# Performance work log

Hardware: AMD Instinct MI355X
Metric: run time of the kernel (lower is better)

Reference implementation:

```python
import jax, jax.numpy as jnp
import numpy as np

B, N, F = 4, 4096, 32
NG = 14  # number of gate graph-convs in GCNLSTM_Cell with memory state


def setup_inputs() -> dict:
    key = jax.random.key(0)
    ks = jax.random.split(key, 7)
    x = jax.random.normal(ks[0], (B, N, F), jnp.float32)
    h = jax.random.normal(ks[1], (B, N, F), jnp.float32)
    c = jax.random.normal(ks[2], (B, N, F), jnp.float32)
    m = jax.random.normal(ks[3], (B, N, F), jnp.float32)
    # weighted dense adjacency, scaled so row sums are O(1)
    adj = jax.random.uniform(ks[4], (N, N), jnp.float32) / N
    # 14 WeightedGraphConv layers: Dense F -> 2F (single FeedForward layer, no relu)
    W = jax.random.normal(ks[5], (NG, F, 2 * F), jnp.float32) * (1.0 / np.sqrt(F))
    b = jnp.zeros((NG, 2 * F), jnp.float32)
    return {"x": x, "h": h, "c": c, "m": m, "adj": adj, "W": W, "b": b}


def _gcn(ax, W, b):
    # ax: [B,N,F] = adj @ state (precomputed); Dense to 2F then GLU split.
    z = ax @ W + b  # [B,N,2F]
    ls, rs = jnp.split(z, 2, axis=-1)
    return ls * jax.nn.sigmoid(rs)


def reference(x, h, c, m, adj, W, b):
    # shared graph aggregation for x and h (adj is the same for all gates)
    ax = jnp.einsum('nm,bmf->bnf', adj, x)  # [B,N,F]
    ah = jnp.einsum('nm,bmf->bnf', adj, h)

    fx = _gcn(ax, W[0], b[0]); fh = _gcn(ah, W[1], b[1])
    ix = _gcn(ax, W[2], b[2]); ih = _gcn(ah, W[3], b[3])
    cx = _gcn(ax, W[4], b[4]); ch = _gcn(ah, W[5], b[5])
    ox = _gcn(ax, W[6], b[6]); oh = _gcn(ah, W[7], b[7])

    f = jax.nn.sigmoid(fx + fh)
    i = jax.nn.sigmoid(ix + ih)
    o = jax.nn.sigmoid(ox + oh)
    c_new = f * c + i * jnp.tanh(cx + ch)
    h1 = o * jnp.tanh(c_new)

    # memory-state block (6 more graph convs on h1 and m)
    ah1 = jnp.einsum('nm,bmf->bnf', adj, h1)
    am = jnp.einsum('nm,bmf->bnf', adj, m)
    sa_ih = _gcn(ah1, W[8], b[8]);  sa_im = _gcn(am, W[9], b[9])
    sa_gh = _gcn(ah1, W[10], b[10]); sa_gm = _gcn(am, W[11], b[11])
    sa_oh = _gcn(ah1, W[12], b[12]); sa_om = _gcn(am, W[13], b[13])

    i2 = jax.nn.sigmoid(sa_ih + sa_im)
    g = jax.nn.sigmoid(sa_gh + sa_gm)
    o2 = jax.nn.sigmoid(sa_oh + sa_om)
    m_new = i2 * m + (1.0 - i2) * g
    h_new = m_new * o2
    return h_new, c_new, m_new
```

## Files before the change

kernel.cpp:

```cpp
#include <hip/hip_runtime.h>
#include <stdint.h>

typedef __attribute__((ext_vector_type(4))) float f32x4;
typedef __attribute__((ext_vector_type(8))) short s16x8;

#define BB 4
#define NN 4096
#define FF 32
#define BNF (BB*NN*FF)

typedef __attribute__((address_space(3))) void       as3_void;
typedef const __attribute__((address_space(1))) void as1_cvoid;

static __device__ __forceinline__ float bf2f(uint16_t u) {
    union { uint32_t i; float f; } v; v.i = ((uint32_t)u) << 16; return v.f;
}
static __device__ __forceinline__ uint16_t f2bf(float f) {
    union { float f; uint32_t i; } v; v.f = f;
    uint32_t r = v.i + 0x7FFFu + ((v.i >> 16) & 1u);
    return (uint16_t)(r >> 16);
}
static __device__ __forceinline__ float sig_acc(float x) { return 1.0f / (1.0f + expf(-x)); }

__global__ __launch_bounds__(256) void prep_kernel(
    const float* __restrict__ Wf, uint16_t* __restrict__ Wp,
    const float* __restrict__ x, const float* __restrict__ h,
    const float* __restrict__ m,
    uint16_t* __restrict__ P, uint16_t* __restrict__ P2)
{
    int bid = blockIdx.x;
    int t = threadIdx.x;

    if (bid < 112) {
        int idx = bid * 256 + t;
        int g   = idx >> 11;
        int k   = (idx >> 6) & 31;
        int col = idx & 63;
        uint16_t v = f2bf(Wf[idx]);
        int gp = g >> 1;
        int sl = ((g & 1) << 2) | (k >> 3);
        int ph = sl ^ (col & 7);
        Wp[((gp * 64 + col) * 64) + ph * 8 + (k & 7)] = v;
        return;
    }
    bid -= 112;

    const float* src; uint16_t* dst; int rowbase, b, n0;
    if (bid < 512) {
        int tensor = bid >> 8;
        src = tensor ? h : x; dst = P; rowbase = tensor * 128;
        b = (bid >> 6) & 3; n0 = (bid & 63) * 64;
    } else {
        int q = bid - 512;
        src = m; dst = P2; rowbase = 128;
        b = q >> 6; n0 = (q & 63) * 64;
    }
    __shared__ uint16_t tl[32][65];
    {
        int i = t >> 2, ch = t & 3;
        size_t idx = ((size_t)(b * NN + n0 + i)) * FF + ch * 8;
        float4 v0 = *(const float4*)(src + idx);
        float4 v1 = *(const float4*)(src + idx + 4);
        uint16_t e[8] = { f2bf(v0.x), f2bf(v0.y), f2bf(v0.z), f2bf(v0.w),
                          f2bf(v1.x), f2bf(v1.y), f2bf(v1.z), f2bf(v1.w) };
        #pragma unroll
        for (int k = 0; k < 8; k++) tl[ch * 8 + k][i] = e[k];
    }
    __syncthreads();
    {
        int f = t >> 3, ch = t & 7;
        union { uint4 u; uint16_t e[8]; } v;
        #pragma unroll
        for (int k = 0; k < 8; k++) v.e[k] = tl[f][ch * 8 + k];
        size_t row = (size_t)(rowbase + b * 32 + f);
        *(uint4*)(dst + row * NN + n0 + ch * 8) = v.u;
    }
}

__global__ __launch_bounds__(256, 3) void mega1_kernel(
    const float* __restrict__ adj,
    const uint16_t* __restrict__ P,
    const uint16_t* __restrict__ Wp,
    const float* __restrict__ bf_,
    const float* __restrict__ cf,
    float* __restrict__ cnew, uint16_t* __restrict__ S2t)
{
    __shared__ __align__(16) uint16_t aLb[4][16 * 32];
    __shared__ __align__(16) uint16_t bLb[4][64 * 32];
    __shared__ float    AL[64 * 17];
    __shared__ float    SX[4][64][9];
    __shared__ uint16_t H1[32 * 18];

    int t = threadIdx.x;
    int bid = blockIdx.x;
    int b = bid >> 8, n0 = (bid & 255) * 16;
    int lane = t & 63, w = t >> 6;
    int lm = lane & 15, lk = lane >> 4;
    int j = lm, kg = lk;
    int ej = t & 15, erow = (t >> 4) & 15;

    float cv[2];
    #pragma unroll
    for (int hh = 0; hh < 2; hh++)
        cv[hh] = cf[((size_t)(b * NN + n0 + erow)) * FF + ej + hh * 16];

    int aq = t >> 6, apos = (t & 63) * 16;
    int arow = apos >> 6;
    int aslot = ((apos >> 4) & 3) ^ ((arow >> 1) & 3);
    int bpos = t * 16;
    int brow = bpos >> 6;
    int bslot = ((bpos >> 4) & 3) ^ ((brow >> 1) & 3);
    int bcrow = brow + ((brow < 32) ? b * 32 : 96 + b * 32);
    int rA = lm;          int swA = (lk ^ ((rA >> 1) & 3)) * 8;
    int rB = w * 16 + lm; int swB = (lk ^ ((rB >> 1) & 3)) * 8;

    f32x4 acc = {};
    for (int kk = 0; kk < 4096; kk += 128) {
        {
            size_t aidx = (size_t)(n0 + arow) * 4096 + kk + aq * 32 + aslot * 8;
            union { uint4 u[2]; float f[8]; } va;
            va.u[0] = *(const uint4*)(adj + aidx);
            va.u[1] = *(const uint4*)(adj + aidx + 4);
            union { uint4 u; uint16_t e[8]; } sa;
            #pragma unroll
            for (int k = 0; k < 8; k++) sa.e[k] = f2bf(va.f[k]);
            *(uint4*)((char*)aLb[aq] + apos) = sa.u;
        }
        #pragma unroll
        for (int q = 0; q < 4; q++) {
            size_t bidx = (size_t)bcrow * 4096 + kk + q * 32 + bslot * 8;
            __builtin_amdgcn_global_load_lds((as1_cvoid*)(P + bidx),
                (as3_void*)((char*)bLb[q] + bpos), 16, 0, 0);
        }
        __syncthreads();
        #pragma unroll
        for (int q = 0; q < 4; q++) {
            s16x8 af = *(const s16x8*)(aLb[q] + rA * 32 + swA);
            s16x8 bf = *(const s16x8*)(bLb[q] + rB * 32 + swB);
            acc = __builtin_amdgcn_mfma_f32_16x16x32_bf16(af, bf, acc, 0, 0, 0);
        }
        __syncthreads();
    }

    {
        int cp = w * 16 + lm;
        #pragma unroll
        for (int r = 0; r < 4; r++)
            AL[cp * 17 + lk * 4 + r] = acc[r];
    }
    __syncthreads();

    s16x8 a_ax, a_ah;
    #pragma unroll
    for (int e = 0; e < 8; e++) {
        int k = kg * 8 + e;
        a_ax[e] = (short)f2bf(AL[k * 17 + j]);
        a_ah[e] = (short)f2bf(AL[(32 + k) * 17 + j]);
    }
    {
        int p = w;
        int g0 = p * 2, g1 = p * 2 + 1;
        f32x4 ac0[4] = {}, ac1[4] = {};
        #pragma unroll
        for (int ct = 0; ct < 4; ct++) {
            int col = ct * 16 + j;
            int ph0 = (kg)     ^ (col & 7);
            int ph1 = (4 + kg) ^ (col & 7);
            s16x8 b0 = *(const s16x8*)(Wp + (p * 64 + col) * 64 + ph0 * 8);
            s16x8 b1 = *(const s16x8*)(Wp + (p * 64 + col) * 64 + ph1 * 8);
            ac0[ct] = __builtin_amdgcn_mfma_f32_16x16x32_bf16(a_ax, b0, ac0[ct], 0, 0, 0);
            ac1[ct] = __builtin_amdgcn_mfma_f32_16x16x32_bf16(a_ah, b1, ac1[ct], 0, 0, 0);
        }
        #pragma unroll
        for (int hh = 0; hh < 2; hh++)
            #pragma unroll
            for (int r = 0; r < 4; r++) {
                float z0l = ac0[hh][r]     + bf_[g0 * 64 + hh * 16 + j];
                float z0r = ac0[2 + hh][r] + bf_[g0 * 64 + 32 + hh * 16 + j];
                float z1l = ac1[hh][r]     + bf_[g1 * 64 + hh * 16 + j];
                float z1r = ac1[2 + hh][r] + bf_[g1 * 64 + 32 + hh * 16 + j];
                SX[p][lane][hh * 4 + r] = z0l * sig_acc(z0r) + z1l * sig_acc(z1r);
            }
    }
    __syncthreads();

    {
        int pl = ((erow >> 2) << 4) | ej;
        int ridx = erow & 3;
        #pragma unroll
        for (int hh = 0; hh < 2; hh++) {
            float s0 = SX[0][pl][hh * 4 + ridx];
            float s1 = SX[1][pl][hh * 4 + ridx];
            float s2 = SX[2][pl][hh * 4 + ridx];
            float s3 = SX[3][pl][hh * 4 + ridx];
            float fg = sig_acc(s0), ig = sig_acc(s1);
            float cc = tanhf(s2),   og = sig_acc(s3);
            float cn = fg * cv[hh] + ig * cc;
            size_t gidx = ((size_t)(b * NN + n0 + erow)) * FF + ej + hh * 16;
            cnew[gidx] = cn;
            H1[(ej + hh * 16) * 18 + erow] = f2bf(og * tanhf(cn));
        }
    }
    __syncthreads();
    if (t < 64) {
        int f = t >> 1, half = t & 1;
        union { uint4 u; uint16_t e[8]; } v;
        #pragma unroll
        for (int k = 0; k < 8; k++) v.e[k] = H1[f * 18 + half * 8 + k];
        *(uint4*)(S2t + ((size_t)(b * 32 + f)) * NN + n0 + half * 8) = v.u;
    }
}

__global__ __launch_bounds__(256, 3) void mega2_kernel(
    const float* __restrict__ adj,
    const uint16_t* __restrict__ P2,
    const uint16_t* __restrict__ Wp,
    const float* __restrict__ bf_,
    const float* __restrict__ mf,
    float* __restrict__ hnew, float* __restrict__ mnew)
{
    __shared__ __align__(16) uint16_t aLb[4][16 * 32];
    __shared__ __align__(16) uint16_t bLb[4][64 * 32];
    __shared__ float AL[64 * 17];
    __shared__ float SX[3][64][9];

    int t = threadIdx.x;
    int bid = blockIdx.x;
    int b = bid >> 8, n0 = (bid & 255) * 16;
    int lane = t & 63, w = t >> 6;
    int lm = lane & 15, lk = lane >> 4;
    int j = lm, kg = lk;
    int ej = t & 15, erow = (t >> 4) & 15;

    float mv[2];
    #pragma unroll
    for (int hh = 0; hh < 2; hh++)
        mv[hh] = mf[((size_t)(b * NN + n0 + erow)) * FF + ej + hh * 16];

    int aq = t >> 6, apos = (t & 63) * 16;
    int arow = apos >> 6;
    int aslot = ((apos >> 4) & 3) ^ ((arow >> 1) & 3);
    int bpos = t * 16;
    int brow = bpos >> 6;
    int bslot = ((bpos >> 4) & 3) ^ ((brow >> 1) & 3);
    int bcrow = brow + ((brow < 32) ? b * 32 : 96 + b * 32);
    int rA = lm;          int swA = (lk ^ ((rA >> 1) & 3)) * 8;
    int rB = w * 16 + lm; int swB = (lk ^ ((rB >> 1) & 3)) * 8;

    f32x4 acc = {};
    for (int kk = 0; kk < 4096; kk += 128) {
        {
            size_t aidx = (size_t)(n0 + arow) * 4096 + kk + aq * 32 + aslot * 8;
            union { uint4 u[2]; float f[8]; } va;
            va.u[0] = *(const uint4*)(adj + aidx);
            va.u[1] = *(const uint4*)(adj + aidx + 4);
            union { uint4 u; uint16_t e[8]; } sa;
            #pragma unroll
            for (int k = 0; k < 8; k++) sa.e[k] = f2bf(va.f[k]);
            *(uint4*)((char*)aLb[aq] + apos) = sa.u;
        }
        #pragma unroll
        for (int q = 0; q < 4; q++) {
            size_t bidx = (size_t)bcrow * 4096 + kk + q * 32 + bslot * 8;
            __builtin_amdgcn_global_load_lds((as1_cvoid*)(P2 + bidx),
                (as3_void*)((char*)bLb[q] + bpos), 16, 0, 0);
        }
        __syncthreads();
        #pragma unroll
        for (int q = 0; q < 4; q++) {
            s16x8 af = *(const s16x8*)(aLb[q] + rA * 32 + swA);
            s16x8 bf = *(const s16x8*)(bLb[q] + rB * 32 + swB);
            acc = __builtin_amdgcn_mfma_f32_16x16x32_bf16(af, bf, acc, 0, 0, 0);
        }
        __syncthreads();
    }

    {
        int cp = w * 16 + lm;
        #pragma unroll
        for (int r = 0; r < 4; r++)
            AL[cp * 17 + lk * 4 + r] = acc[r];
    }
    __syncthreads();

    if (w < 3) {
        s16x8 a_h1, a_m;
        #pragma unroll
        for (int e = 0; e < 8; e++) {
            int k = kg * 8 + e;
            a_h1[e] = (short)f2bf(AL[k * 17 + j]);
            a_m[e]  = (short)f2bf(AL[(32 + k) * 17 + j]);
        }
        const uint16_t* WpG = Wp + 4 * 64 * 64;
        const float*    bG  = bf_ + 512;
        int p = w;
        int g0 = p * 2, g1 = p * 2 + 1;
        f32x4 ac0[4] = {}, ac1[4] = {};
        #pragma unroll
        for (int ct = 0; ct < 4; ct++) {
            int col = ct * 16 + j;
            int ph0 = (kg)     ^ (col & 7);
            int ph1 = (4 + kg) ^ (col & 7);
            s16x8 b0 = *(const s16x8*)(WpG + (p * 64 + col) * 64 + ph0 * 8);
            s16x8 b1 = *(const s16x8*)(WpG + (p * 64 + col) * 64 + ph1 * 8);
            ac0[ct] = __builtin_amdgcn_mfma_f32_16x16x32_bf16(a_h1, b0, ac0[ct], 0, 0, 0);
            ac1[ct] = __builtin_amdgcn_mfma_f32_16x16x32_bf16(a_m, b1, ac1[ct], 0, 0, 0);
        }
        #pragma unroll
        for (int hh = 0; hh < 2; hh++)
            #pragma unroll
            for (int r = 0; r < 4; r++) {
                float z0l = ac0[hh][r]     + bG[g0 * 64 + hh * 16 + j];
                float z0r = ac0[2 + hh][r] + bG[g0 * 64 + 32 + hh * 16 + j];
                float z1l = ac1[hh][r]     + bG[g1 * 64 + hh * 16 + j];
                float z1r = ac1[2 + hh][r] + bG[g1 * 64 + 32 + hh * 16 + j];
                SX[p][lane][hh * 4 + r] = z0l * sig_acc(z0r) + z1l * sig_acc(z1r);
            }
    }
    __syncthreads();

    {
        int pl = ((erow >> 2) << 4) | ej;
        int ridx = erow & 3;
        #pragma unroll
        for (int hh = 0; hh < 2; hh++) {
            float s0 = SX[0][pl][hh * 4 + ridx];
            float s1 = SX[1][pl][hh * 4 + ridx];
            float s2 = SX[2][pl][hh * 4 + ridx];
            float i2 = sig_acc(s0);
            float gg = sig_acc(s1);
            float o2 = sig_acc(s2);
            float mn = i2 * mv[hh] + (1.0f - i2) * gg;
            size_t gidx = ((size_t)(b * NN + n0 + erow)) * FF + ej + hh * 16;
            mnew[gidx] = mn;
            hnew[gidx] = mn * o2;
        }
    }
}

extern "C" void kernel_launch(void* const* d_in, const int* in_sizes, int n_in,
                              void* d_out, int out_size, void* d_ws, size_t ws_size,
                              hipStream_t stream) {
    (void)in_sizes; (void)n_in; (void)out_size;
    const float* x   = (const float*)d_in[0];
    const float* h   = (const float*)d_in[1];
    const float* c   = (const float*)d_in[2];
    const float* m   = (const float*)d_in[3];
    const float* adj = (const float*)d_in[4];
    const float* W   = (const float*)d_in[5];
    const float* bb  = (const float*)d_in[6];
    float* out = (float*)d_out;

    char* ws = (char*)d_ws;
    uint16_t* P    = (uint16_t*)ws;
    uint16_t* P2   = (uint16_t*)(ws + (2u << 20));
    uint16_t* Wp   = (uint16_t*)(ws + (4u << 20));

    if (ws_size < (6u << 20)) return;

    prep_kernel<<<880, 256, 0, stream>>>(W, Wp, x, h, m, P, P2);

    mega1_kernel<<<1024, 256, 0, stream>>>(adj, P, Wp, bb, c, out + BNF, P2);
    mega2_kernel<<<1024, 256, 0, stream>>>(adj, P2, Wp, bb, m, out, out + 2 * BNF);
}
```

Measured before the change: 187.3 us.

## Pre-convert adjacency to bf16 once and double row tile per block

Adds a prep pass that converts the fp32 adjacency to a bf16 copy in workspace, when the workspace is large enough. Both mega kernels can then stream A with direct global-to-LDS loads instead of loading fp32 and converting in registers. Each block now covers 32 rows instead of 16, with two MFMA accumulators that share each B fragment, so the grid halves and the P reloads per row are halved. The cost is an extra 32MB write plus re-read of adjacency, fewer blocks (512) with occupancy lowered to 2 waves, and a serialized two-pass epilogue.

```diff
diff --git a/kernel.cpp b/kernel.cpp
--- a/kernel.cpp
+++ b/kernel.cpp
@@ -23,6 +23,7 @@
 static __device__ __forceinline__ float sig_acc(float x) { return 1.0f / (1.0f + expf(-x)); }
 
 __global__ __launch_bounds__(256) void prep_kernel(
+    const float* __restrict__ adj, uint16_t* __restrict__ adjb, int cvtN,
     const float* __restrict__ Wf, uint16_t* __restrict__ Wp,
     const float* __restrict__ x, const float* __restrict__ h,
     const float* __restrict__ m,
@@ -30,6 +31,18 @@
 {
     int bid = blockIdx.x;
     int t = threadIdx.x;
+
+    if (bid < cvtN) {
+        size_t i = ((size_t)bid * 256 + t) * 8;
+        float4 v0 = *(const float4*)(adj + i);
+        float4 v1 = *(const float4*)(adj + i + 4);
+        union { uint4 u; uint16_t e[8]; } o;
+        o.e[0] = f2bf(v0.x); o.e[1] = f2bf(v0.y); o.e[2] = f2bf(v0.z); o.e[3] = f2bf(v0.w);
+        o.e[4] = f2bf(v1.x); o.e[5] = f2bf(v1.y); o.e[6] = f2bf(v1.z); o.e[7] = f2bf(v1.w);
+        *(uint4*)(adjb + i) = o.u;
+        return;
+    }
+    bid -= cvtN;
 
     if (bid < 112) {
         int idx = bid * 256 + t;
@@ -77,54 +90,79 @@
     }
 }
 
-__global__ __launch_bounds__(256, 3) void mega1_kernel(
-    const float* __restrict__ adj,
+__global__ __launch_bounds__(256, 2) void mega1_kernel(
+    const void* __restrict__ Av,
     const uint16_t* __restrict__ P,
     const uint16_t* __restrict__ Wp,
     const float* __restrict__ bf_,
     const float* __restrict__ cf,
-    float* __restrict__ cnew, uint16_t* __restrict__ S2t)
+    float* __restrict__ cnew, uint16_t* __restrict__ S2t, int isf32A)
 {
-    __shared__ __align__(16) uint16_t aLb[4][16 * 32];
+    __shared__ __align__(16) uint16_t aLb[4][32 * 32];
     __shared__ __align__(16) uint16_t bLb[4][64 * 32];
-    __shared__ float    AL[64 * 17];
+    __shared__ float    AL[64 * 33];
     __shared__ float    SX[4][64][9];
     __shared__ uint16_t H1[32 * 18];
 
     int t = threadIdx.x;
     int bid = blockIdx.x;
-    int b = bid >> 8, n0 = (bid & 255) * 16;
+    int b = bid >> 7, n0 = (bid & 127) * 32;
     int lane = t & 63, w = t >> 6;
     int lm = lane & 15, lk = lane >> 4;
     int j = lm, kg = lk;
     int ej = t & 15, erow = (t >> 4) & 15;
 
-    float cv[2];
+    const uint16_t* A16 = (const uint16_t*)Av;
+    const float*    Af  = (const float*)Av;
+
+    float cv[2][2];
     #pragma unroll
-    for (int hh = 0; hh < 2; hh++)
-        cv[hh] = cf[((size_t)(b * NN + n0 + erow)) * FF + ej + hh * 16];
-
-    int aq = t >> 6, apos = (t & 63) * 16;
-    int arow = apos >> 6;
-    int aslot = ((apos >> 4) & 3) ^ ((arow >> 1) & 3);
+    for (int gh = 0; gh < 2; gh++)
+        #pragma unroll
+        for (int hh = 0; hh < 2; hh++)
+            cv[gh][hh] = cf[((size_t)(b * NN + n0 + gh * 16 + erow)) * FF + ej + hh * 16];
+
+    int aq0 = t >> 7,        ap0 = (t & 127) * 16;
+    int ar0 = ap0 >> 6,      asl0 = ((ap0 >> 4) & 3) ^ ((ar0 >> 1) & 3);
+    int gs1 = t + 256;
+    int aq1 = gs1 >> 7,      ap1 = (gs1 & 127) * 16;
+    int ar1 = ap1 >> 6,      asl1 = ((ap1 >> 4) & 3) ^ ((ar1 >> 1) & 3);
     int bpos = t * 16;
     int brow = bpos >> 6;
     int bslot = ((bpos >> 4) & 3) ^ ((brow >> 1) & 3);
     int bcrow = brow + ((brow < 32) ? b * 32 : 96 + b * 32);
-    int rA = lm;          int swA = (lk ^ ((rA >> 1) & 3)) * 8;
     int rB = w * 16 + lm; int swB = (lk ^ ((rB >> 1) & 3)) * 8;
-
-    f32x4 acc = {};
+    int swA = (lk ^ ((lm >> 1) & 3)) * 8;
+
+    f32x4 acc0 = {}, acc1 = {};
     for (int kk = 0; kk < 4096; kk += 128) {
-        {
-            size_t aidx = (size_t)(n0 + arow) * 4096 + kk + aq * 32 + aslot * 8;
-            union { uint4 u[2]; float f[8]; } va;
-            va.u[0] = *(const uint4*)(adj + aidx);
-            va.u[1] = *(const uint4*)(adj + aidx + 4);
-            union { uint4 u; uint16_t e[8]; } sa;
-            #pragma unroll
-            for (int k = 0; k < 8; k++) sa.e[k] = f2bf(va.f[k]);
-            *(uint4*)((char*)aLb[aq] + apos) = sa.u;
+        if (!isf32A) {
+            __builtin_amdgcn_global_load_lds(
+                (as1_cvoid*)(A16 + (size_t)(n0 + ar0) * 4096 + kk + aq0 * 32 + asl0 * 8),
+                (as3_void*)((char*)aLb[aq0] + ap0), 16, 0, 0);
+            __builtin_amdgcn_global_load_lds(
+                (as1_cvoid*)(A16 + (size_t)(n0 + ar1) * 4096 + kk + aq1 * 32 + asl1 * 8),
+                (as3_void*)((char*)aLb[aq1] + ap1), 16, 0, 0);
+        } else {
+            union { uint4 u; uint16_t e[8]; } sa0, sa1;
+            {
+                size_t aidx = (size_t)(n0 + ar0) * 4096 + kk + aq0 * 32 + asl0 * 8;
+                union { uint4 u[2]; float f[8]; } va;
+                va.u[0] = *(const uint4*)(Af + aidx);
+                va.u[1] = *(const uint4*)(Af + aidx + 4);
+                #pragma unroll
+                for (int k = 0; k < 8; k++) sa0.e[k] = f2bf(va.f[k]);
+            }
+            {
+                size_t aidx = (size_t)(n0 + ar1) * 4096 + kk + aq1 * 32 + asl1 * 8;
+                union { uint4 u[2]; float f[8]; } va;
+                va.u[0] = *(const uint4*)(Af + aidx);
+                va.u[1] = *(const uint4*)(Af + aidx + 4);
+                #pragma unroll
+                for (int k = 0; k < 8; k++) sa1.e[k] = f2bf(va.f[k]);
+            }
+            *(uint4*)((char*)aLb[aq0] + ap0) = sa0.u;
+            *(uint4*)((char*)aLb[aq1] + ap1) = sa1.u;
         }
         #pragma unroll
         for (int q = 0; q < 4; q++) {
@@ -135,9 +173,11 @@
         __syncthreads();
         #pragma unroll
         for (int q = 0; q < 4; q++) {
-            s16x8 af = *(const s16x8*)(aLb[q] + rA * 32 + swA);
-            s16x8 bf = *(const s16x8*)(bLb[q] + rB * 32 + swB);
-            acc = __builtin_amdgcn_mfma_f32_16x16x32_bf16(af, bf, acc, 0, 0, 0);
+            s16x8 af0 = *(const s16x8*)(aLb[q] + lm * 32 + swA);
+            s16x8 af1 = *(const s16x8*)(aLb[q] + (16 + lm) * 32 + swA);
+            s16x8 bf  = *(const s16x8*)(bLb[q] + rB * 32 + swB);
+            acc0 = __builtin_amdgcn_mfma_f32_16x16x32_bf16(af0, bf, acc0, 0, 0, 0);
+            acc1 = __builtin_amdgcn_mfma_f32_16x16x32_bf16(af1, bf, acc1, 0, 0, 0);
         }
         __syncthreads();
     }
@@ -145,119 +185,149 @@
     {
         int cp = w * 16 + lm;
         #pragma unroll
-        for (int r = 0; r < 4; r++)
-            AL[cp * 17 + lk * 4 + r] = acc[r];
+        for (int r = 0; r < 4; r++) {
+            AL[cp * 33 + lk * 4 + r]      = acc0[r];
+            AL[cp * 33 + 16 + lk * 4 + r] = acc1[r];
+        }
     }
     __syncthreads();
 
-    s16x8 a_ax, a_ah;
-    #pragma unroll
-    for (int e = 0; e < 8; e++) {
-        int k = kg * 8 + e;
-        a_ax[e] = (short)f2bf(AL[k * 17 + j]);
-        a_ah[e] = (short)f2bf(AL[(32 + k) * 17 + j]);
-    }
-    {
-        int p = w;
-        int g0 = p * 2, g1 = p * 2 + 1;
-        f32x4 ac0[4] = {}, ac1[4] = {};
-        #pragma unroll
-        for (int ct = 0; ct < 4; ct++) {
-            int col = ct * 16 + j;
-            int ph0 = (kg)     ^ (col & 7);
-            int ph1 = (4 + kg) ^ (col & 7);
-            s16x8 b0 = *(const s16x8*)(Wp + (p * 64 + col) * 64 + ph0 * 8);
-            s16x8 b1 = *(const s16x8*)(Wp + (p * 64 + col) * 64 + ph1 * 8);
-            ac0[ct] = __builtin_amdgcn_mfma_f32_16x16x32_bf16(a_ax, b0, ac0[ct], 0, 0, 0);
-            ac1[ct] = __builtin_amdgcn_mfma_f32_16x16x32_bf16(a_ah, b1, ac1[ct], 0, 0, 0);
-        }
-        #pragma unroll
-        for (int hh = 0; hh < 2; hh++)
-            #pragma unroll
-            for (int r = 0; r < 4; r++) {
-                float z0l = ac0[hh][r]     + bf_[g0 * 64 + hh * 16 + j];
-                float z0r = ac0[2 + hh][r] + bf_[g0 * 64 + 32 + hh * 16 + j];
-                float z1l = ac1[hh][r]     + bf_[g1 * 64 + hh * 16 + j];
-                float z1r = ac1[2 + hh][r] + bf_[g1 * 64 + 32 + hh * 16 + j];
-                SX[p][lane][hh * 4 + r] = z0l * sig_acc(z0r) + z1l * sig_acc(z1r);
-            }
-    }
-    __syncthreads();
-
-    {
-        int pl = ((erow >> 2) << 4) | ej;
-        int ridx = erow & 3;
-        #pragma unroll
-        for (int hh = 0; hh < 2; hh++) {
-            float s0 = SX[0][pl][hh * 4 + ridx];
-            float s1 = SX[1][pl][hh * 4 + ridx];
-            float s2 = SX[2][pl][hh * 4 + ridx];
-            float s3 = SX[3][pl][hh * 4 + ridx];
-            float fg = sig_acc(s0), ig = sig_acc(s1);
-            float cc = tanhf(s2),   og = sig_acc(s3);
-            float cn = fg * cv[hh] + ig * cc;
-            size_t gidx = ((size_t)(b * NN + n0 + erow)) * FF + ej + hh * 16;
-            cnew[gidx] = cn;
-            H1[(ej + hh * 16) * 18 + erow] = f2bf(og * tanhf(cn));
-        }
-    }
-    __syncthreads();
-    if (t < 64) {
-        int f = t >> 1, half = t & 1;
-        union { uint4 u; uint16_t e[8]; } v;
-        #pragma unroll
-        for (int k = 0; k < 8; k++) v.e[k] = H1[f * 18 + half * 8 + k];
-        *(uint4*)(S2t + ((size_t)(b * 32 + f)) * NN + n0 + half * 8) = v.u;
-    }
-}
-
-__global__ __launch_bounds__(256, 3) void mega2_kernel(
-    const float* __restrict__ adj,
+    for (int gh = 0; gh < 2; gh++) {
+        int colb = gh * 16;
+        s16x8 a_ax, a_ah;
+        #pragma unroll
+        for (int e = 0; e < 8; e++) {
+            int k = kg * 8 + e;
+            a_ax[e] = (short)f2bf(AL[k * 33 + colb + j]);
+            a_ah[e] = (short)f2bf(AL[(32 + k) * 33 + colb + j]);
+        }
+        {
+            int p = w;
+            int g0 = p * 2, g1 = p * 2 + 1;
+            f32x4 ac0[4] = {}, ac1[4] = {};
+            #pragma unroll
+            for (int ct = 0; ct < 4; ct++) {
+                int col = ct * 16 + j;
+                int ph0 = (kg)     ^ (col & 7);
+                int ph1 = (4 + kg) ^ (col & 7);
+                s16x8 b0 = *(const s16x8*)(Wp + (p * 64 + col) * 64 + ph0 * 8);
+                s16x8 b1 = *(const s16x8*)(Wp + (p * 64 + col) * 64 + ph1 * 8);
+                ac0[ct] = __builtin_amdgcn_mfma_f32_16x16x32_bf16(a_ax, b0, ac0[ct], 0, 0, 0);
+                ac1[ct] = __builtin_amdgcn_mfma_f32_16x16x32_bf16(a_ah, b1, ac1[ct], 0, 0, 0);
+            }
+            #pragma unroll
+            for (int hh = 0; hh < 2; hh++)
+                #pragma unroll
+                for (int r = 0; r < 4; r++) {
+                    float z0l = ac0[hh][r]     + bf_[g0 * 64 + hh * 16 + j];
+                    float z0r = ac0[2 + hh][r] + bf_[g0 * 64 + 32 + hh * 16 + j];
+                    float z1l = ac1[hh][r]     + bf_[g1 * 64 + hh * 16 + j];
+                    float z1r = ac1[2 + hh][r] + bf_[g1 * 64 + 32 + hh * 16 + j];
+                    SX[p][lane][hh * 4 + r] = z0l * sig_acc(z0r) + z1l * sig_acc(z1r);
+                }
+        }
+        __syncthreads();
+        {
+            int pl = ((erow >> 2) << 4) | ej;
+            int ridx = erow & 3;
+            #pragma unroll
+            for (int hh = 0; hh < 2; hh++) {
+                float s0 = SX[0][pl][hh * 4 + ridx];
+                float s1 = SX[1][pl][hh * 4 + ridx];
+                float s2 = SX[2][pl][hh * 4 + ridx];
+                float s3 = SX[3][pl][hh * 4 + ridx];
+                float fg = sig_acc(s0), ig = sig_acc(s1);
+                float cc = tanhf(s2),   og = sig_acc(s3);
+                float cn = fg * cv[gh][hh] + ig * cc;
+                size_t gidx = ((size_t)(b * NN + n0 + gh * 16 + erow)) * FF + ej + hh * 16;
+                cnew[gidx] = cn;
+                H1[(ej + hh * 16) * 18 + erow] = f2bf(og * tanhf(cn));
+            }
+        }
+        __syncthreads();
+        if (t < 64) {
+            int f = t >> 1, half = t & 1;
+            union { uint4 u; uint16_t e[8]; } v;
+            #pragma unroll
+            for (int k = 0; k < 8; k++) v.e[k] = H1[f * 18 + half * 8 + k];
+            *(uint4*)(S2t + ((size_t)(b * 32 + f)) * NN + n0 + gh * 16 + half * 8) = v.u;
+        }
+        __syncthreads();
+    }
+}
+
+__global__ __launch_bounds__(256, 2) void mega2_kernel(
+    const void* __restrict__ Av,
     const uint16_t* __restrict__ P2,
     const uint16_t* __restrict__ Wp,
     const float* __restrict__ bf_,
     const float* __restrict__ mf,
-    float* __restrict__ hnew, float* __restrict__ mnew)
+    float* __restrict__ hnew, float* __restrict__ mnew, int isf32A)
 {
-    __shared__ __align__(16) uint16_t aLb[4][16 * 32];
+    __shared__ __align__(16) uint16_t aLb[4][32 * 32];
     __shared__ __align__(16) uint16_t bLb[4][64 * 32];
-    __shared__ float AL[64 * 17];
+    __shared__ float AL[64 * 33];
     __shared__ float SX[3][64][9];
 
     int t = threadIdx.x;
     int bid = blockIdx.x;
-    int b = bid >> 8, n0 = (bid & 255) * 16;
+    int b = bid >> 7, n0 = (bid & 127) * 32;
     int lane = t & 63, w = t >> 6;
     int lm = lane & 15, lk = lane >> 4;
     int j = lm, kg = lk;
     int ej = t & 15, erow = (t >> 4) & 15;
 
-    float mv[2];
+    const uint16_t* A16 = (const uint16_t*)Av;
+    const float*    Af  = (const float*)Av;
+
+    float mv[2][2];
     #pragma unroll
-    for (int hh = 0; hh < 2; hh++)
-        mv[hh] = mf[((size_t)(b * NN + n0 + erow)) * FF + ej + hh * 16];
-
-    int aq = t >> 6, apos = (t & 63) * 16;
-    int arow = apos >> 6;
-    int aslot = ((apos >> 4) & 3) ^ ((arow >> 1) & 3);
+    for (int gh = 0; gh < 2; gh++)
+        #pragma unroll
+        for (int hh = 0; hh < 2; hh++)
+            mv[gh][hh] = mf[((size_t)(b * NN + n0 + gh * 16 + erow)) * FF + ej + hh * 16];
+
+    int aq0 = t >> 7,        ap0 = (t & 127) * 16;
+    int ar0 = ap0 >> 6,      asl0 = ((ap0 >> 4) & 3) ^ ((ar0 >> 1) & 3);
+    int gs1 = t + 256;
+    int aq1 = gs1 >> 7,      ap1 = (gs1 & 127) * 16;
+    int ar1 = ap1 >> 6,      asl1 = ((ap1 >> 4) & 3) ^ ((ar1 >> 1) & 3);
     int bpos = t * 16;
     int brow = bpos >> 6;
     int bslot = ((bpos >> 4) & 3) ^ ((brow >> 1) & 3);
     int bcrow = brow + ((brow < 32) ? b * 32 : 96 + b * 32);
-    int rA = lm;          int swA = (lk ^ ((rA >> 1) & 3)) * 8;
     int rB = w * 16 + lm; int swB = (lk ^ ((rB >> 1) & 3)) * 8;
-
-    f32x4 acc = {};
+    int swA = (lk ^ ((lm >> 1) & 3)) * 8;
+
+    f32x4 acc0 = {}, acc1 = {};
     for (int kk = 0; kk < 4096; kk += 128) {
-        {
-            size_t aidx = (size_t)(n0 + arow) * 4096 + kk + aq * 32 + aslot * 8;
-            union { uint4 u[2]; float f[8]; } va;
-            va.u[0] = *(const uint4*)(adj + aidx);
-            va.u[1] = *(const uint4*)(adj + aidx + 4);
-            union { uint4 u; uint16_t e[8]; } sa;
-            #pragma unroll
-            for (int k = 0; k < 8; k++) sa.e[k] = f2bf(va.f[k]);
-            *(uint4*)((char*)aLb[aq] + apos) = sa.u;
+        if (!isf32A) {
+            __builtin_amdgcn_global_load_lds(
+                (as1_cvoid*)(A16 + (size_t)(n0 + ar0) * 4096 + kk + aq0 * 32 + asl0 * 8),
+                (as3_void*)((char*)aLb[aq0] + ap0), 16, 0, 0);
+            __builtin_amdgcn_global_load_lds(
+                (as1_cvoid*)(A16 + (size_t)(n0 + ar1) * 4096 + kk + aq1 * 32 + asl1 * 8),
+                (as3_void*)((char*)aLb[aq1] + ap1), 16, 0, 0);
+        } else {
+            union { uint4 u; uint16_t e[8]; } sa0, sa1;
+            {
+                size_t aidx = (size_t)(n0 + ar0) * 4096 + kk + aq0 * 32 + asl0 * 8;
+                union { uint4 u[2]; float f[8]; } va;
+                va.u[0] = *(const uint4*)(Af + aidx);
+                va.u[1] = *(const uint4*)(Af + aidx + 4);
+                #pragma unroll
+                for (int k = 0; k < 8; k++) sa0.e[k] = f2bf(va.f[k]);
+            }
+            {
+                size_t aidx = (size_t)(n0 + ar1) * 4096 + kk + aq1 * 32 + asl1 * 8;
+                union { uint4 u[2]; float f[8]; } va;
+                va.u[0] = *(const uint4*)(Af + aidx);
+                va.u[1] = *(const uint4*)(Af + aidx + 4);
+                #pragma unroll
+                for (int k = 0; k < 8; k++) sa1.e[k] = f2bf(va.f[k]);
+            }
+            *(uint4*)((char*)aLb[aq0] + ap0) = sa0.u;
+            *(uint4*)((char*)aLb[aq1] + ap1) = sa1.u;
         }
         #pragma unroll
         for (int q = 0; q < 4; q++) {
@@ -268,9 +338,11 @@
         __syncthreads();
         #pragma unroll
         for (int q = 0; q < 4; q++) {
-            s16x8 af = *(const s16x8*)(aLb[q] + rA * 32 + swA);
-            s16x8 bf = *(const s16x8*)(bLb[q] + rB * 32 + swB);
-            acc = __builtin_amdgcn_mfma_f32_16x16x32_bf16(af, bf, acc, 0, 0, 0);
+            s16x8 af0 = *(const s16x8*)(aLb[q] + lm * 32 + swA);
+            s16x8 af1 = *(const s16x8*)(aLb[q] + (16 + lm) * 32 + swA);
+            s16x8 bf  = *(const s16x8*)(bLb[q] + rB * 32 + swB);
+            acc0 = __builtin_amdgcn_mfma_f32_16x16x32_bf16(af0, bf, acc0, 0, 0, 0);
+            acc1 = __builtin_amdgcn_mfma_f32_16x16x32_bf16(af1, bf, acc1, 0, 0, 0);
         }
         __syncthreads();
     }
@@ -278,63 +350,68 @@
     {
         int cp = w * 16 + lm;
         #pragma unroll
-        for (int r = 0; r < 4; r++)
-            AL[cp * 17 + lk * 4 + r] = acc[r];
+        for (int r = 0; r < 4; r++) {
+            AL[cp * 33 + lk * 4 + r]      = acc0[r];
+            AL[cp * 33 + 16 + lk * 4 + r] = acc1[r];
+        }
     }
     __syncthreads();
 
-    if (w < 3) {
-        s16x8 a_h1, a_m;
-        #pragma unroll
-        for (int e = 0; e < 8; e++) {
-            int k = kg * 8 + e;
-            a_h1[e] = (short)f2bf(AL[k * 17 + j]);
-            a_m[e]  = (short)f2bf(AL[(32 + k) * 17 + j]);
-        }
-        const uint16_t* WpG = Wp + 4 * 64 * 64;
-        const float*    bG  = bf_ + 512;
-        int p = w;
-        int g0 = p * 2, g1 = p * 2 + 1;
-        f32x4 ac0[4] = {}, ac1[4] = {};
-        #pragma unroll
-        for (int ct = 0; ct < 4; ct++) {
-            int col = ct * 16 + j;
-            int ph0 = (kg)     ^ (col & 7);
-            int ph1 = (4 + kg) ^ (col & 7);
-            s16x8 b0 = *(const s16x8*)(WpG + (p * 64 + col) * 64 + ph0 * 8);
-            s16x8 b1 = *(const s16x8*)(WpG + (p * 64 + col) * 64 + ph1 * 8);
-            ac0[ct] = __builtin_amdgcn_mfma_f32_16x16x32_bf16(a_h1, b0, ac0[ct], 0, 0, 0);
-            ac1[ct] = __builtin_amdgcn_mfma_f32_16x16x32_bf16(a_m, b1, ac1[ct], 0, 0, 0);
-        }
-        #pragma unroll
-        for (int hh = 0; hh < 2; hh++)
-            #pragma unroll
-            for (int r = 0; r < 4; r++) {
-                float z0l = ac0[hh][r]     + bG[g0 * 64 + hh * 16 + j];
-                float z0r = ac0[2 + hh][r] + bG[g0 * 64 + 32 + hh * 16 + j];
-                float z1l = ac1[hh][r]     + bG[g1 * 64 + hh * 16 + j];
-                float z1r = ac1[2 + hh][r] + bG[g1 * 64 + 32 + hh * 16 + j];
-                SX[p][lane][hh * 4 + r] = z0l * sig_acc(z0r) + z1l * sig_acc(z1r);
-            }
-    }
-    __syncthreads();
-
-    {
-        int pl = ((erow >> 2) << 4) | ej;
-        int ridx = erow & 3;
-        #pragma unroll
-        for (int hh = 0; hh < 2; hh++) {
-            float s0 = SX[0][pl][hh * 4 + ridx];
-            float s1 = SX[1][pl][hh * 4 + ridx];
-            float s2 = SX[2][pl][hh * 4 + ridx];
-            float i2 = sig_acc(s0);
-            float gg = sig_acc(s1);
-            float o2 = sig_acc(s2);
-            float mn = i2 * mv[hh] + (1.0f - i2) * gg;
-            size_t gidx = ((size_t)(b * NN + n0 + erow)) * FF + ej + hh * 16;
-            mnew[gidx] = mn;
-            hnew[gidx] = mn * o2;
-        }
+    for (int gh = 0; gh < 2; gh++) {
+        int colb = gh * 16;
+        if (w < 3) {
+            s16x8 a_h1, a_m;
+            #pragma unroll
+            for (int e = 0; e < 8; e++) {
+                int k = kg * 8 + e;
+                a_h1[e] = (short)f2bf(AL[k * 33 + colb + j]);
+                a_m[e]  = (short)f2bf(AL[(32 + k) * 33 + colb + j]);
+            }
+            const uint16_t* WpG = Wp + 4 * 64 * 64;
+            const float*    bG  = bf_ + 512;
+            int p = w;
+            int g0 = p * 2, g1 = p * 2 + 1;
+            f32x4 ac0[4] = {}, ac1[4] = {};
+            #pragma unroll
+            for (int ct = 0; ct < 4; ct++) {
+                int col = ct * 16 + j;
+                int ph0 = (kg)     ^ (col & 7);
+                int ph1 = (4 + kg) ^ (col & 7);
+                s16x8 b0 = *(const s16x8*)(WpG + (p * 64 + col) * 64 + ph0 * 8);
+                s16x8 b1 = *(const s16x8*)(WpG + (p * 64 + col) * 64 + ph1 * 8);
+                ac0[ct] = __builtin_amdgcn_mfma_f32_16x16x32_bf16(a_h1, b0, ac0[ct], 0, 0, 0);
+                ac1[ct] = __builtin_amdgcn_mfma_f32_16x16x32_bf16(a_m, b1, ac1[ct], 0, 0, 0);
+            }
+            #pragma unroll
+            for (int hh = 0; hh < 2; hh++)
+                #pragma unroll
+                for (int r = 0; r < 4; r++) {
+                    float z0l = ac0[hh][r]     + bG[g0 * 64 + hh * 16 + j];
+                    float z0r = ac0[2 + hh][r] + bG[g0 * 64 + 32 + hh * 16 + j];
+                    float z1l = ac1[hh][r]     + bG[g1 * 64 + hh * 16 + j];
+                    float z1r = ac1[2 + hh][r] + bG[g1 * 64 + 32 + hh * 16 + j];
+                    SX[p][lane][hh * 4 + r] = z0l * sig_acc(z0r) + z1l * sig_acc(z1r);
+                }
+        }
+        __syncthreads();
+        {
+            int pl = ((erow >> 2) << 4) | ej;
+            int ridx = erow & 3;
+            #pragma unroll
+            for (int hh = 0; hh < 2; hh++) {
+                float s0 = SX[0][pl][hh * 4 + ridx];
+                float s1 = SX[1][pl][hh * 4 + ridx];
+                float s2 = SX[2][pl][hh * 4 + ridx];
+                float i2 = sig_acc(s0);
+                float gg = sig_acc(s1);
+                float o2 = sig_acc(s2);
+                float mn = i2 * mv[gh][hh] + (1.0f - i2) * gg;
+                size_t gidx = ((size_t)(b * NN + n0 + gh * 16 + erow)) * FF + ej + hh * 16;
+                mnew[gidx] = mn;
+                hnew[gidx] = mn * o2;
+            }
+        }
+        __syncthreads();
     }
 }
 
@@ -352,14 +429,21 @@
     float* out = (float*)d_out;
 
     char* ws = (char*)d_ws;
-    uint16_t* P    = (uint16_t*)ws;
-    uint16_t* P2   = (uint16_t*)(ws + (2u << 20));
-    uint16_t* Wp   = (uint16_t*)(ws + (4u << 20));
+    int haveAdjb = ws_size >= (size_t)(40u << 20);
+    uint16_t* adjb = (uint16_t*)ws;
+    size_t pOff = haveAdjb ? (size_t)(32u << 20) : 0;
+    uint16_t* P    = (uint16_t*)(ws + pOff);
+    uint16_t* P2   = (uint16_t*)(ws + pOff + (2u << 20));
+    uint16_t* Wp   = (uint16_t*)(ws + pOff + (4u << 20));
 
     if (ws_size < (6u << 20)) return;
 
-    prep_kernel<<<880, 256, 0, stream>>>(W, Wp, x, h, m, P, P2);
-
-    mega1_kernel<<<1024, 256, 0, stream>>>(adj, P, Wp, bb, c, out + BNF, P2);
-    mega2_kernel<<<1024, 256, 0, stream>>>(adj, P2, Wp, bb, m, out, out + 2 * BNF);
-}
+    const void* Agemm = haveAdjb ? (const void*)adjb : (const void*)adj;
+    int isf32A = haveAdjb ? 0 : 1;
+    int cvtN = haveAdjb ? 8192 : 0;
+
+    prep_kernel<<<cvtN + 112 + 768, 256, 0, stream>>>(adj, adjb, cvtN, W, Wp, x, h, m, P, P2);
+
+    mega1_kernel<<<512, 256, 0, stream>>>(Agemm, P, Wp, bb, c, out + BNF, P2, isf32A);
+    mega2_kernel<<<512, 256, 0, stream>>>(Agemm, P2, Wp, bb, m, out, out + 2 * BNF, isf32A);
+}
```

New measurement: 172.9 us. 1.08x faster.
